# Performance work log

Measured on AMD Instinct MI355X. Metric: run time of the kernel, lower is better.

## Reference

```python
import jax, jax.numpy as jnp
import numpy as np

B, L, W = 512, 1024, 256


def setup_inputs() -> dict:
    key = jax.random.key(0)
    ks = jax.random.split(key, 7)
    # spin configurations in {-1, +1}
    x = (jax.random.randint(ks[0], (B, L), 0, 2).astype(jnp.float32) * 2.0 - 1.0)
    s = 0.1  # param init scale
    w_ih = jax.random.normal(ks[1], (3 * W, 2), jnp.float32) * s
    w_hh = jax.random.normal(ks[2], (3 * W, W), jnp.float32) * s
    b_ih = jax.random.normal(ks[3], (3 * W,), jnp.float32) * s
    b_hh = jax.random.normal(ks[4], (3 * W,), jnp.float32) * s
    fc_w = jax.random.normal(ks[5], (2, W), jnp.float32) * s
    fc_b = jax.random.normal(ks[6], (2,), jnp.float32) * s
    return {"x": x, "w_ih": w_ih, "w_hh": w_hh, "b_ih": b_ih,
            "b_hh": b_hh, "fc_w": fc_w, "fc_b": fc_b}


def reference(x, w_ih, w_hh, b_ih, b_hh, fc_w, fc_b):
    b, n = x.shape
    w = w_hh.shape[1]
    mask = (1.0 + x) * 0.5                                   # [B, L]
    # input to step i is x[:, i-1]; step 0 uses x_init = 0 (embeds to [0.5, 0.5])
    xs = jnp.concatenate([jnp.zeros((b, 1), x.dtype), x[:, :-1]], axis=1)
    emb = jnp.stack([(xs + 1.0) * 0.5, 1.0 - (xs + 1.0) * 0.5], axis=-1)  # [B, L, 2]
    # precompute all input-side gate projections in one GEMM: [B, L, 3W]
    gi_all = jnp.einsum('blk,gk->blg', emb, w_ih) + b_ih

    def step(h, inp):
        gi, m = inp                                          # [B,3W], [B]
        gh = h @ w_hh.T + b_hh                               # [B,3W]
        i_r, i_z, i_n = jnp.split(gi, 3, axis=1)
        h_r, h_z, h_n = jnp.split(gh, 3, axis=1)
        r = jax.nn.sigmoid(i_r + h_r)
        z = jax.nn.sigmoid(i_z + h_z)
        ng = jnp.tanh(i_n + r * h_n)
        h_next = (1.0 - z) * ng + z * h                      # torch GRUCell update
        y = jax.nn.log_softmax(h_next @ fc_w.T + fc_b, axis=1)  # [B,2]
        lp = y[:, 0] * m + y[:, 1] * (1.0 - m)
        return h_next, lp

    gi_t = jnp.swapaxes(gi_all, 0, 1)                        # [L, B, 3W]
    m_t = mask.T                                             # [L, B]
    h0 = jnp.zeros((b, w), x.dtype)
    _, lps = jax.lax.scan(step, h0, (gi_t, m_t))             # lps: [L, B]
    return lps.sum(axis=0)                                   # [B]
```

## Files before the change

### kernel.cpp

```cpp
#include <hip/hip_runtime.h>
#include <math.h>

#define SL 1024
#define NW 256

typedef _Float16 half8 __attribute__((ext_vector_type(8)));
typedef _Float16 half2t __attribute__((ext_vector_type(2)));
typedef float f32x4 __attribute__((ext_vector_type(4)));

__device__ __forceinline__ float rcp_f(float v) { return __builtin_amdgcn_rcpf(v); }

__global__ __launch_bounds__(512, 2) void gru_mfma_kernel(
    const float* __restrict__ x, const float* __restrict__ w_ih,
    const float* __restrict__ w_hh, const float* __restrict__ b_ih,
    const float* __restrict__ b_hh, const float* __restrict__ fc_w,
    const float* __restrict__ fc_b, float* __restrict__ out)
{
    const int tid  = threadIdx.x;
    const int w    = tid >> 6;
    const int lane = tid & 63;
    const int c    = lane & 15;
    const int g    = lane >> 4;
    const int gl   = g & 1;
    const int row  = g >> 1;
    const int row0 = blockIdx.x * 2;

    __shared__ float    x_lds[2][1026];
    __shared__ __align__(16) _Float16 h_lds[2][2][288];
    __shared__ float    dpart[SL][8][2];
    __shared__ float    wsum[8][2];

    for (int i = tid; i < 2 * SL; i += 512) {
        int b = i >> 10, j = i & (SL - 1);
        x_lds[b][1 + j] = (x[(size_t)(row0 + b) * SL + j] + 1.0f) * 0.5f;
    }
    if (tid < 2) x_lds[tid][0] = 0.5f;
    for (int i = tid; i < 2 * 2 * 288; i += 512)
        ((_Float16*)h_lds)[i] = (_Float16)0.0f;

    half8 Bf[6][8];
    #pragma unroll
    for (int f = 0; f < 6; ++f) {
        const int q = f >> 1, jt = f & 1;
        const int urow = q * NW + (2 * w + jt) * 16 + c;
        #pragma unroll
        for (int j = 0; j < 8; ++j) {
            const int ktp = (w + j) & 7;
            const float* p = w_hh + (size_t)urow * NW + ktp * 32 + g * 8;
            float4 lo = *(const float4*)p;
            float4 hi = *(const float4*)(p + 4);
            half8 hb;
            hb[0] = (_Float16)lo.x; hb[1] = (_Float16)lo.y;
            hb[2] = (_Float16)lo.z; hb[3] = (_Float16)lo.w;
            hb[4] = (_Float16)hi.x; hb[5] = (_Float16)hi.y;
            hb[6] = (_Float16)hi.z; hb[7] = (_Float16)hi.w;
            Bf[f][j] = hb;
        }
    }

    half8 B7 = (half8)(_Float16)0.0f;
    if (c == 0) {
        #pragma unroll
        for (int e = 0; e < 8; ++e) {
            const int k = w * 32 + g * 8 + e;
            B7[e] = (_Float16)(fc_w[k] - fc_w[NW + k]);
        }
    }

    const int u = 32 * w + 16 * gl + c;
    half2t pkr, pkz, pkn;
    {
        float w0, w1;
        w0 = w_ih[2 * u]; w1 = w_ih[2 * u + 1];
        pkr[0] = (_Float16)(w1 + b_ih[u] + b_hh[u]);
        pkr[1] = (_Float16)(w0 - w1);
        w0 = w_ih[2 * (NW + u)]; w1 = w_ih[2 * (NW + u) + 1];
        pkz[0] = (_Float16)(w1 + b_ih[NW + u] + b_hh[NW + u]);
        pkz[1] = (_Float16)(w0 - w1);
        w0 = w_ih[2 * (2 * NW + u)]; w1 = w_ih[2 * (2 * NW + u) + 1];
        pkn[0] = (_Float16)(w1 + b_ih[2 * NW + u]);
        pkn[1] = (_Float16)(w0 - w1);
    }
    const float bhn = b_hh[2 * NW + u];
    const float bd  = fc_b[0] - fc_b[1];

    const f32x4 zc = {0.f, 0.f, 0.f, 0.f};
    float h0 = 0.f;

    f32x4 acc[6];
    #pragma unroll
    for (int f = 0; f < 6; ++f) acc[f] = zc;
    f32x4 acc7 = zc;

    __syncthreads();

    #pragma unroll 1
    for (int t = 0; t < SL; ++t) {
        const int cur = t & 1, nxt = cur ^ 1;

        if (lane == 0 && t != 0) {
            dpart[t - 1][w][0] = acc7[0];
            dpart[t - 1][w][1] = acc7[1];
        }

        const _Float16* hb = &h_lds[cur][lane & 1][g * 8];
        #pragma unroll
        for (int j = 1; j < 8; ++j) {
            const int ktp = (w + j) & 7;
            half8 A = *(const half8*)(hb + ktp * 32);
            #pragma unroll
            for (int f = 0; f < 6; ++f)
                acc[f] = __builtin_amdgcn_mfma_f32_16x16x32_f16(A, Bf[f][j], acc[f], 0, 0, 0);
        }

        const float m  = x_lds[row][t];
        const float ar = row ? (gl ? acc[1][1] : acc[0][1]) : (gl ? acc[1][0] : acc[0][0]);
        const float az = row ? (gl ? acc[3][1] : acc[2][1]) : (gl ? acc[3][0] : acc[2][0]);
        const float an = row ? (gl ? acc[5][1] : acc[4][1]) : (gl ? acc[5][0] : acc[4][0]);

        const float cmr = (float)pkr[0], cdr = (float)pkr[1];
        const float cmz = (float)pkz[0], cdz = (float)pkz[1];
        const float cmn = (float)pkn[0], cdn = (float)pkn[1];

        const float vr = ar + fmaf(m, cdr, cmr);
        const float rr = rcp_f(1.f + __expf(-vr));
        const float vz = az + fmaf(m, cdz, cmz);
        const float zz = rcp_f(1.f + __expf(-vz));
        const float un = fmaf(rr, an + bhn, fmaf(m, cdn, cmn));
        const float ng = fmaf(-2.f, rcp_f(1.f + __expf(2.f * un)), 1.f);
        const float hn = fmaf(zz, h0 - ng, ng);
        h0 = hn;

        h_lds[nxt][row][u] = (_Float16)hn;

        {
            half8 A = *(const half8*)&h_lds[nxt][lane & 1][w * 32 + g * 8];
            #pragma unroll
            for (int f = 0; f < 6; ++f)
                acc[f] = __builtin_amdgcn_mfma_f32_16x16x32_f16(A, Bf[f][0], zc, 0, 0, 0);
            acc7 = __builtin_amdgcn_mfma_f32_16x16x32_f16(A, B7, zc, 0, 0, 0);
        }

        __syncthreads();
    }

    if (lane == 0) {
        dpart[SL - 1][w][0] = acc7[0];
        dpart[SL - 1][w][1] = acc7[1];
    }
    __syncthreads();

    float lpp0 = 0.f, lpp1 = 0.f;
    #pragma unroll 1
    for (int t = tid; t < SL; t += 512) {
        float d0 = bd, d1 = bd;
        #pragma unroll
        for (int q = 0; q < 8; ++q) { d0 += dpart[t][q][0]; d1 += dpart[t][q][1]; }
        const float u0 = (x_lds[0][t + 1] > 0.5f) ? -d0 : d0;
        const float u1 = (x_lds[1][t + 1] > 0.5f) ? -d1 : d1;
        lpp0 -= fmaxf(u0, 0.f) + __logf(1.f + __expf(-fabsf(u0)));
        lpp1 -= fmaxf(u1, 0.f) + __logf(1.f + __expf(-fabsf(u1)));
    }
    #pragma unroll
    for (int s = 1; s < 64; s <<= 1) {
        lpp0 += __shfl_xor(lpp0, s);
        lpp1 += __shfl_xor(lpp1, s);
    }
    if (lane == 0) { wsum[w][0] = lpp0; wsum[w][1] = lpp1; }
    __syncthreads();
    if (tid < 2) {
        float s = 0.f;
        #pragma unroll
        for (int q = 0; q < 8; ++q) s += wsum[q][tid];
        out[row0 + tid] = s;
    }
}

extern "C" void kernel_launch(void* const* d_in, const int* in_sizes, int n_in,
                              void* d_out, int out_size, void* d_ws, size_t ws_size,
                              hipStream_t stream) {
    const float* x    = (const float*)d_in[0];
    const float* w_ih = (const float*)d_in[1];
    const float* w_hh = (const float*)d_in[2];
    const float* b_ih = (const float*)d_in[3];
    const float* b_hh = (const float*)d_in[4];
    const float* fc_w = (const float*)d_in[5];
    const float* fc_b = (const float*)d_in[6];
    gru_mfma_kernel<<<256, 512, 0, stream>>>(
        x, w_ih, w_hh, b_ih, b_hh, fc_w, fc_b, (float*)d_out);
}
```

Before: 1.060 ms.

## Compute output projection via lane shuffles and drop early own-slice MFMA

Removes the extra MFMA with the fc weight tile (B7) and instead computes the per-step output logit difference as a scalar product per lane, reduced with xor-shuffles across 32 lanes. It also stops issuing the wave's own k-slice MFMAs right after writing h, before the barrier. All eight k-tiles are now computed after the barrier, in natural order. This frees registers and one MFMA per step, but puts six more MFMAs on the serial critical path after each barrier and adds shuffle latency each step.

```diff
diff --git a/kernel.cpp b/kernel.cpp
--- a/kernel.cpp
+++ b/kernel.cpp
@@ -44,9 +44,8 @@
         const int q = f >> 1, jt = f & 1;
         const int urow = q * NW + (2 * w + jt) * 16 + c;
         #pragma unroll
-        for (int j = 0; j < 8; ++j) {
-            const int ktp = (w + j) & 7;
-            const float* p = w_hh + (size_t)urow * NW + ktp * 32 + g * 8;
+        for (int kt = 0; kt < 8; ++kt) {
+            const float* p = w_hh + (size_t)urow * NW + kt * 32 + g * 8;
             float4 lo = *(const float4*)p;
             float4 hi = *(const float4*)(p + 4);
             half8 hb;
@@ -54,21 +53,12 @@
             hb[2] = (_Float16)lo.z; hb[3] = (_Float16)lo.w;
             hb[4] = (_Float16)hi.x; hb[5] = (_Float16)hi.y;
             hb[6] = (_Float16)hi.z; hb[7] = (_Float16)hi.w;
-            Bf[f][j] = hb;
-        }
-    }
-
-    half8 B7 = (half8)(_Float16)0.0f;
-    if (c == 0) {
-        #pragma unroll
-        for (int e = 0; e < 8; ++e) {
-            const int k = w * 32 + g * 8 + e;
-            B7[e] = (_Float16)(fc_w[k] - fc_w[NW + k]);
+            Bf[f][kt] = hb;
         }
     }
 
     const int u = 32 * w + 16 * gl + c;
-    half2t pkr, pkz, pkn;
+    half2t pkr, pkz, pkn, pkh;
     {
         float w0, w1;
         w0 = w_ih[2 * u]; w1 = w_ih[2 * u + 1];
@@ -80,17 +70,13 @@
         w0 = w_ih[2 * (2 * NW + u)]; w1 = w_ih[2 * (2 * NW + u) + 1];
         pkn[0] = (_Float16)(w1 + b_ih[2 * NW + u]);
         pkn[1] = (_Float16)(w0 - w1);
+        pkh[0] = (_Float16)b_hh[2 * NW + u];
+        pkh[1] = (_Float16)(fc_w[u] - fc_w[NW + u]);
     }
-    const float bhn = b_hh[2 * NW + u];
-    const float bd  = fc_b[0] - fc_b[1];
 
     const f32x4 zc = {0.f, 0.f, 0.f, 0.f};
     float h0 = 0.f;
-
-    f32x4 acc[6];
-    #pragma unroll
-    for (int f = 0; f < 6; ++f) acc[f] = zc;
-    f32x4 acc7 = zc;
+    float p_prev = 0.f;
 
     __syncthreads();
 
@@ -98,19 +84,28 @@
     for (int t = 0; t < SL; ++t) {
         const int cur = t & 1, nxt = cur ^ 1;
 
-        if (lane == 0 && t != 0) {
-            dpart[t - 1][w][0] = acc7[0];
-            dpart[t - 1][w][1] = acc7[1];
+        {
+            float p = p_prev;
+            p += __shfl_xor(p, 1);  p += __shfl_xor(p, 2);
+            p += __shfl_xor(p, 4);  p += __shfl_xor(p, 8);
+            p += __shfl_xor(p, 16);
+            if (t != 0 && (lane & 31) == 0) dpart[t - 1][w][row] = p;
         }
 
+        f32x4 acc[6];
         const _Float16* hb = &h_lds[cur][lane & 1][g * 8];
-        #pragma unroll
-        for (int j = 1; j < 8; ++j) {
-            const int ktp = (w + j) & 7;
-            half8 A = *(const half8*)(hb + ktp * 32);
+        {
+            half8 A = *(const half8*)(hb);
             #pragma unroll
             for (int f = 0; f < 6; ++f)
-                acc[f] = __builtin_amdgcn_mfma_f32_16x16x32_f16(A, Bf[f][j], acc[f], 0, 0, 0);
+                acc[f] = __builtin_amdgcn_mfma_f32_16x16x32_f16(A, Bf[f][0], zc, 0, 0, 0);
+        }
+        #pragma unroll
+        for (int kt = 1; kt < 8; ++kt) {
+            half8 A = *(const half8*)(hb + kt * 32);
+            #pragma unroll
+            for (int f = 0; f < 6; ++f)
+                acc[f] = __builtin_amdgcn_mfma_f32_16x16x32_f16(A, Bf[f][kt], acc[f], 0, 0, 0);
         }
 
         const float m  = x_lds[row][t];
@@ -118,38 +113,32 @@
         const float az = row ? (gl ? acc[3][1] : acc[2][1]) : (gl ? acc[3][0] : acc[2][0]);
         const float an = row ? (gl ? acc[5][1] : acc[4][1]) : (gl ? acc[5][0] : acc[4][0]);
 
-        const float cmr = (float)pkr[0], cdr = (float)pkr[1];
-        const float cmz = (float)pkz[0], cdz = (float)pkz[1];
-        const float cmn = (float)pkn[0], cdn = (float)pkn[1];
-
-        const float vr = ar + fmaf(m, cdr, cmr);
+        const float vr = ar + fmaf(m, (float)pkr[1], (float)pkr[0]);
         const float rr = rcp_f(1.f + __expf(-vr));
-        const float vz = az + fmaf(m, cdz, cmz);
+        const float vz = az + fmaf(m, (float)pkz[1], (float)pkz[0]);
         const float zz = rcp_f(1.f + __expf(-vz));
-        const float un = fmaf(rr, an + bhn, fmaf(m, cdn, cmn));
+        const float un = fmaf(rr, an + (float)pkh[0], fmaf(m, (float)pkn[1], (float)pkn[0]));
         const float ng = fmaf(-2.f, rcp_f(1.f + __expf(2.f * un)), 1.f);
         const float hn = fmaf(zz, h0 - ng, ng);
         h0 = hn;
 
         h_lds[nxt][row][u] = (_Float16)hn;
 
-        {
-            half8 A = *(const half8*)&h_lds[nxt][lane & 1][w * 32 + g * 8];
-            #pragma unroll
-            for (int f = 0; f < 6; ++f)
-                acc[f] = __builtin_amdgcn_mfma_f32_16x16x32_f16(A, Bf[f][0], zc, 0, 0, 0);
-            acc7 = __builtin_amdgcn_mfma_f32_16x16x32_f16(A, B7, zc, 0, 0, 0);
-        }
+        p_prev = hn * (float)pkh[1];
 
         __syncthreads();
     }
 
-    if (lane == 0) {
-        dpart[SL - 1][w][0] = acc7[0];
-        dpart[SL - 1][w][1] = acc7[1];
+    {
+        float p = p_prev;
+        p += __shfl_xor(p, 1);  p += __shfl_xor(p, 2);
+        p += __shfl_xor(p, 4);  p += __shfl_xor(p, 8);
+        p += __shfl_xor(p, 16);
+        if ((lane & 31) == 0) dpart[SL - 1][w][row] = p;
     }
     __syncthreads();
 
+    const float bd = fc_b[0] - fc_b[1];
     float lpp0 = 0.f, lpp1 = 0.f;
     #pragma unroll 1
     for (int t = tid; t < SL; t += 512) {
```

Result: slower. 1.100 ms (+3.8%).
